# Kernel optimization log

Measured on AMD Instinct MI355X. Metric: run time of the kernel, lower is better.

## Reference

```python
import jax, jax.numpy as jnp
import numpy as np

ALPHA = 0.2  # LeakyReLU negative slope used by GAT attention


def _seg_softmax(scores, rows, n):
    # numerically stable softmax of per-edge scores grouped by destination row
    m = jax.ops.segment_max(scores, rows, num_segments=n)
    ex = jnp.exp(scores - m[rows])
    s = jax.ops.segment_sum(ex, rows, num_segments=n)
    return ex / s[rows]


def setup_inputs() -> dict:
    key = jax.random.key(0)
    ks = jax.random.split(key, 10)
    VOCAB, U, N, DEG = 200000, 50000, 20000, 16
    DIN, DOUT, H, ETYPES, EDIM = 64, 64, 4, 32, 64
    node_features = jax.random.normal(ks[0], (VOCAB, DIN), jnp.float32)
    W = jax.random.normal(ks[1], (H, DIN, DOUT), jnp.float32) * np.float32(np.sqrt(2.0 / (DIN + DOUT)))
    a_pos = jax.random.normal(ks[2], (H, 2 * DOUT), jnp.float32) * 0.1
    a_neg = jax.random.normal(ks[3], (H, 2 * DOUT), jnp.float32) * 0.1
    edge_embedding = jax.random.normal(ks[4], (ETYPES, EDIM), jnp.float32)
    edge_transform = jax.random.normal(ks[5], (EDIM, DOUT), jnp.float32) * np.float32(np.sqrt(2.0 / (EDIM + DOUT)))
    unique_nodes = jax.random.randint(ks[6], (U,), 0, VOCAB)
    row_unique = jax.random.randint(ks[7], (N,), 0, U)  # index of each output row's own node in the unique list
    # pos adjacency with self edges appended (adj_pos2 in the source)
    pos_row = jnp.concatenate([jnp.repeat(jnp.arange(N), DEG), jnp.arange(N)])
    pos_col = jnp.concatenate([jax.random.randint(ks[8], (N * DEG,), 0, U), row_unique])
    neg_row = jnp.repeat(jnp.arange(N), DEG)
    neg_col = jax.random.randint(ks[9], (N * DEG,), 0, U)
    return {
        "node_features": node_features, "W": W, "a_pos": a_pos, "a_neg": a_neg,
        "edge_embedding": edge_embedding, "edge_transform": edge_transform,
        "unique_nodes": unique_nodes, "row_unique": row_unique,
        "pos_row": pos_row, "pos_col": pos_col, "neg_row": neg_row, "neg_col": neg_col,
        "n_rows": N,
    }


def reference(node_features, W, a_pos, a_neg, edge_embedding, edge_transform,
              unique_nodes, row_unique, pos_row, pos_col, neg_row, neg_col, n_rows):
    embed = node_features[unique_nodes]                 # [U, Din] gather of unique node embeddings
    Wh = jnp.einsum('ud,hdo->huo', embed, W)            # [H, U, Dout]
    Dout = W.shape[-1]
    rows_all = jnp.concatenate([pos_row, neg_row])
    cols_all = jnp.concatenate([pos_col, neg_col])

    def head(Wh_h, ap, an):
        # per-node score halves (GAT trick: a^T[h_i || h_j] = a_dst.h_i + a_src.h_j)
        dst_p = (Wh_h @ ap[:Dout])[row_unique]          # [N]
        src_p = Wh_h @ ap[Dout:]                        # [U]
        dst_n = (Wh_h @ an[:Dout])[row_unique]
        src_n = Wh_h @ an[Dout:]
        e_pos = jax.nn.leaky_relu(dst_p[pos_row] + src_p[pos_col], ALPHA)
        e_neg = jax.nn.leaky_relu(dst_n[neg_row] + src_n[neg_col], ALPHA)
        att = _seg_softmax(jnp.concatenate([e_pos, e_neg]), rows_all, n_rows)  # joint softmax over pos+neg edges
        return jax.ops.segment_sum(att[:, None] * Wh_h[cols_all], rows_all, num_segments=n_rows)

    outs = jax.vmap(head)(Wh, a_pos, a_neg)             # [H, N, Dout]
    h_hidden = jax.nn.relu(jnp.transpose(outs, (1, 0, 2)).reshape(outs.shape[1], -1))  # concat heads -> ReLU
    edge_out = edge_embedding @ edge_transform          # edge-type projection
    return (h_hidden, edge_out)
```

## Files before the change

### kernel.cpp

```cpp
#include <hip/hip_runtime.h>
#include <hip/hip_bf16.h>
#include <hip/hip_fp16.h>
#include <math.h>

#define LRELU_ALPHA 0.2f

typedef __attribute__((ext_vector_type(8))) short bf16x8;
typedef __attribute__((ext_vector_type(4))) float f32x4;
typedef _Float16 f16x8 __attribute__((ext_vector_type(8)));

__device__ __forceinline__ unsigned short f2bf(float f) {
    union { float f; unsigned u; } v; v.f = f;
    unsigned r = v.u + 0x7fffu + ((v.u >> 16) & 1u);
    return (unsigned short)(r >> 16);
}
__device__ __forceinline__ unsigned short f2h(float f) {
    union { __half h; unsigned short s; } c; c.h = __float2half_rn(f); return c.s;
}
__device__ __forceinline__ unsigned cvtpk(float lo, float hi) {
    unsigned r;
    asm("v_cvt_pk_bf16_f32 %0, %1, %2" : "=v"(r) : "v"(lo), "v"(hi));
    return r;
}
__device__ __forceinline__ __half2 u2h2(unsigned u) {
    union { unsigned u; __half2 h; } x; x.u = u; return x.h;
}
__device__ __forceinline__ unsigned h22u(__half2 h) {
    union { __half2 h; unsigned u; } x; x.h = h; return x.u;
}

__global__ void prep_kernel(const float* __restrict__ W,
                            const float* __restrict__ a_pos, const float* __restrict__ a_neg,
                            const float* __restrict__ ee, const float* __restrict__ et,
                            unsigned short* __restrict__ Wt, unsigned short* __restrict__ avB,
                            float* __restrict__ edge_out, int H, int ET) {
    const int HE = H * 4096, AV = H * 256;
    int t = blockIdx.x * blockDim.x + threadIdx.x;
    if (t < HE) {
        int k = t & 63, n = (t >> 6) & 63, h = t >> 12;
        Wt[((size_t)h * 64 + n) * 64 + k] = f2h(W[(size_t)h * 4096 + k * 64 + n]);
    } else if (t < HE + AV) {
        int s = t - HE;
        int k = s & 63, q = (s >> 6) & 3, h = s >> 8;
        const float* a  = (q < 2 ? a_pos : a_neg) + (size_t)h * 128 + (q & 1) * 64;
        const float* wr = W + (size_t)h * 4096 + k * 64;
        float v = 0.f;
#pragma unroll
        for (int o = 0; o < 64; o += 4) {
            const float4 wv = *(const float4*)(wr + o);
            const float4 av = *(const float4*)(a + o);
            v = fmaf(wv.x, av.x, fmaf(wv.y, av.y, fmaf(wv.z, av.z, fmaf(wv.w, av.w, v))));
        }
        avB[((size_t)h * 4 + q) * 64 + k] = f2bf(v);
    } else {
        int s = t - HE - AV;
        if (s < ET * 64) {
            int e = s >> 6, o = s & 63;
            float acc = 0.f;
#pragma unroll
            for (int k = 0; k < 64; ++k)
                acc = fmaf(ee[e * 64 + k], et[k * 64 + o], acc);
            edge_out[s] = acc;
        }
    }
}

__global__ __launch_bounds__(256) void score_cvt_kernel(
    const float* __restrict__ nf, const unsigned short* __restrict__ avB,
    const int* __restrict__ un, unsigned short* __restrict__ embed16,
    float2* __restrict__ sc_dst, float2* __restrict__ sc_src, int U)
{
    const int wave = threadIdx.x >> 6;
    const int lane = threadIdx.x & 63;
    const int grp  = lane >> 4;
    const int r    = lane & 15;
    const long u0  = (long)blockIdx.x * 64 + wave * 16;
    if (u0 >= U) return;
    const long u  = u0 + r;
    const long ur = (u < U) ? u : (long)(U - 1);

    const float* erow = nf + (size_t)un[ur] * 64 + grp * 8;
    const float4 e0 = *(const float4*)(erow);
    const float4 e1 = *(const float4*)(erow + 4);
    const float4 e2 = *(const float4*)(erow + 32);
    const float4 e3 = *(const float4*)(erow + 36);

    union { unsigned d[4]; bf16x8 v; } A0, A1;
    A0.d[0] = cvtpk(e0.x, e0.y); A0.d[1] = cvtpk(e0.z, e0.w);
    A0.d[2] = cvtpk(e1.x, e1.y); A0.d[3] = cvtpk(e1.z, e1.w);
    A1.d[0] = cvtpk(e2.x, e2.y); A1.d[1] = cvtpk(e2.z, e2.w);
    A1.d[2] = cvtpk(e3.x, e3.y); A1.d[3] = cvtpk(e3.z, e3.w);

    if (u < U) {
        union { __half2 h2[4]; uint4 v; } F0, F1;
        F0.h2[0] = __floats2half2_rn(e0.x, e0.y); F0.h2[1] = __floats2half2_rn(e0.z, e0.w);
        F0.h2[2] = __floats2half2_rn(e1.x, e1.y); F0.h2[3] = __floats2half2_rn(e1.z, e1.w);
        F1.h2[0] = __floats2half2_rn(e2.x, e2.y); F1.h2[1] = __floats2half2_rn(e2.z, e2.w);
        F1.h2[2] = __floats2half2_rn(e3.x, e3.y); F1.h2[3] = __floats2half2_rn(e3.z, e3.w);
        *(uint4*)(embed16 + (size_t)u * 64 + grp * 8)      = F0.v;
        *(uint4*)(embed16 + (size_t)u * 64 + 32 + grp * 8) = F1.v;
    }

    f32x4 acc = (f32x4)(0.f);
    const unsigned short* wp = avB + (size_t)r * 64 + grp * 8;
    bf16x8 b0 = *(const bf16x8*)wp;
    bf16x8 b1 = *(const bf16x8*)(wp + 32);
    acc = __builtin_amdgcn_mfma_f32_16x16x32_bf16(b0, A0.v, acc, 0, 0, 0);
    acc = __builtin_amdgcn_mfma_f32_16x16x32_bf16(b1, A1.v, acc, 0, 0, 0);

    if (u < U) {
        sc_dst[(size_t)u * 4 + grp] = make_float2(acc[0], acc[2]);
        sc_src[(size_t)u * 4 + grp] = make_float2(acc[1], acc[3]);
    }
}

__global__ __launch_bounds__(512) void aggemm_kernel(
    const int* __restrict__ pos_col, const int* __restrict__ neg_col,
    const unsigned short* __restrict__ embed16,
    const float2* __restrict__ sc_dst, const float2* __restrict__ sc_src,
    const unsigned short* __restrict__ Wt,
    float* __restrict__ out, int N, int U)
{
    constexpr int DP = 16, NE = 33, NEP = 36;
    __shared__ int   s_col[8][2][NEP];
    __shared__ uint4 s_att[8][2][NEP];
    __shared__ __align__(16) unsigned short s_agg[16][256];

    const int wave = threadIdx.x >> 6;
    const int lane = threadIdx.x & 63;
    const int iA = blockIdx.x * 16 + wave * 2;
    const int iB = iA + 1;

    int colA = 0, colB = 0;
    if (lane < DP)       { colA = pos_col[(size_t)iA * DP + lane];
                           colB = pos_col[(size_t)iB * DP + lane]; }
    else if (lane == DP) { colA = pos_col[(size_t)N * DP + iA];
                           colB = pos_col[(size_t)N * DP + iB]; }
    else if (lane < NE)  { colA = neg_col[(size_t)iA * 16 + (lane - DP - 1)];
                           colB = neg_col[(size_t)iB * 16 + (lane - DP - 1)]; }

    const float4* ssv = (const float4*)sc_src;
    const float4 sA0 = ssv[2 * (size_t)(unsigned)colA];
    const float4 sA1 = ssv[2 * (size_t)(unsigned)colA + 1];
    const float4 sB0 = ssv[2 * (size_t)(unsigned)colB];
    const float4 sB1 = ssv[2 * (size_t)(unsigned)colB + 1];
    const int uA = __shfl(colA, DP, 64), uB = __shfl(colB, DP, 64);
    const float4* sdv = (const float4*)sc_dst;
    const float4 dA0 = sdv[2 * (size_t)(unsigned)uA];
    const float4 dA1 = sdv[2 * (size_t)(unsigned)uA + 1];
    const float4 dB0 = sdv[2 * (size_t)(unsigned)uB];
    const float4 dB1 = sdv[2 * (size_t)(unsigned)uB + 1];

    const bool isp = (lane <= DP);
    float a_s0 = isp ? dA0.x + sA0.x : dA0.y + sA0.y;
    float a_s1 = isp ? dA0.z + sA0.z : dA0.w + sA0.w;
    float a_s2 = isp ? dA1.x + sA1.x : dA1.y + sA1.y;
    float a_s3 = isp ? dA1.z + sA1.z : dA1.w + sA1.w;
    float b_s0 = isp ? dB0.x + sB0.x : dB0.y + sB0.y;
    float b_s1 = isp ? dB0.z + sB0.z : dB0.w + sB0.w;
    float b_s2 = isp ? dB1.x + sB1.x : dB1.y + sB1.y;
    float b_s3 = isp ? dB1.z + sB1.z : dB1.w + sB1.w;
    a_s0 = (a_s0 > 0.f) ? a_s0 : LRELU_ALPHA * a_s0;
    a_s1 = (a_s1 > 0.f) ? a_s1 : LRELU_ALPHA * a_s1;
    a_s2 = (a_s2 > 0.f) ? a_s2 : LRELU_ALPHA * a_s2;
    a_s3 = (a_s3 > 0.f) ? a_s3 : LRELU_ALPHA * a_s3;
    b_s0 = (b_s0 > 0.f) ? b_s0 : LRELU_ALPHA * b_s0;
    b_s1 = (b_s1 > 0.f) ? b_s1 : LRELU_ALPHA * b_s1;
    b_s2 = (b_s2 > 0.f) ? b_s2 : LRELU_ALPHA * b_s2;
    b_s3 = (b_s3 > 0.f) ? b_s3 : LRELU_ALPHA * b_s3;

    const bool act = (lane < NE);
    float ax0 = act ? __expf(a_s0) : 0.f, ax1 = act ? __expf(a_s1) : 0.f;
    float ax2 = act ? __expf(a_s2) : 0.f, ax3 = act ? __expf(a_s3) : 0.f;
    float bx0 = act ? __expf(b_s0) : 0.f, bx1 = act ? __expf(b_s1) : 0.f;
    float bx2 = act ? __expf(b_s2) : 0.f, bx3 = act ? __expf(b_s3) : 0.f;
    float aS0 = ax0, aS1 = ax1, aS2 = ax2, aS3 = ax3;
    float bS0 = bx0, bS1 = bx1, bS2 = bx2, bS3 = bx3;
#pragma unroll
    for (int off = 32; off; off >>= 1) {
        aS0 += __shfl_xor(aS0, off, 64); aS1 += __shfl_xor(aS1, off, 64);
        aS2 += __shfl_xor(aS2, off, 64); aS3 += __shfl_xor(aS3, off, 64);
        bS0 += __shfl_xor(bS0, off, 64); bS1 += __shfl_xor(bS1, off, 64);
        bS2 += __shfl_xor(bS2, off, 64); bS3 += __shfl_xor(bS3, off, 64);
    }
    if (lane < NEP) {
        uint4 tA, tB;
        tA.x = h22u(__float2half2_rn(__fdividef(ax0, aS0)));
        tA.y = h22u(__float2half2_rn(__fdividef(ax1, aS1)));
        tA.z = h22u(__float2half2_rn(__fdividef(ax2, aS2)));
        tA.w = h22u(__float2half2_rn(__fdividef(ax3, aS3)));
        tB.x = h22u(__float2half2_rn(__fdividef(bx0, bS0)));
        tB.y = h22u(__float2half2_rn(__fdividef(bx1, bS1)));
        tB.z = h22u(__float2half2_rn(__fdividef(bx2, bS2)));
        tB.w = h22u(__float2half2_rn(__fdividef(bx3, bS3)));
        s_col[wave][0][lane] = colA;  s_att[wave][0][lane] = tA;
        s_col[wave][1][lane] = colB;  s_att[wave][1][lane] = tB;
    }

    const int sub = lane >> 4;
    const int c   = lane & 15;
    const char* eb = (const char*)embed16 + (c << 3);
    __half2 accA[4][2], accB[4][2];
#pragma unroll
    for (int h = 0; h < 4; ++h)
        for (int d = 0; d < 2; ++d) {
            accA[h][d] = __float2half2_rn(0.f);
            accB[h][d] = __float2half2_rn(0.f);
        }
#pragma unroll
    for (int t = 0; t < 9; ++t) {
        const int   e  = 4 * t + sub;
        const int   cA = s_col[wave][0][e];
        const int   cB = s_col[wave][1][e];
        const uint2 vA = *(const uint2*)(eb + ((size_t)(unsigned)cA << 7));
        const uint2 vB = *(const uint2*)(eb + ((size_t)(unsigned)cB << 7));
        const uint4 tA = s_att[wave][0][e];
        const uint4 tB = s_att[wave][1][e];
        const __half2 vA0 = u2h2(vA.x), vA1 = u2h2(vA.y);
        const __half2 vB0 = u2h2(vB.x), vB1 = u2h2(vB.y);
        accA[0][0] = __hfma2(u2h2(tA.x), vA0, accA[0][0]);
        accA[0][1] = __hfma2(u2h2(tA.x), vA1, accA[0][1]);
        accA[1][0] = __hfma2(u2h2(tA.y), vA0, accA[1][0]);
        accA[1][1] = __hfma2(u2h2(tA.y), vA1, accA[1][1]);
        accA[2][0] = __hfma2(u2h2(tA.z), vA0, accA[2][0]);
        accA[2][1] = __hfma2(u2h2(tA.z), vA1, accA[2][1]);
        accA[3][0] = __hfma2(u2h2(tA.w), vA0, accA[3][0]);
        accA[3][1] = __hfma2(u2h2(tA.w), vA1, accA[3][1]);
        accB[0][0] = __hfma2(u2h2(tB.x), vB0, accB[0][0]);
        accB[0][1] = __hfma2(u2h2(tB.x), vB1, accB[0][1]);
        accB[1][0] = __hfma2(u2h2(tB.y), vB0, accB[1][0]);
        accB[1][1] = __hfma2(u2h2(tB.y), vB1, accB[1][1]);
        accB[2][0] = __hfma2(u2h2(tB.z), vB0, accB[2][0]);
        accB[2][1] = __hfma2(u2h2(tB.z), vB1, accB[2][1]);
        accB[3][0] = __hfma2(u2h2(tB.w), vB0, accB[3][0]);
        accB[3][1] = __hfma2(u2h2(tB.w), vB1, accB[3][1]);
    }
#pragma unroll
    for (int h = 0; h < 4; ++h)
#pragma unroll
        for (int d = 0; d < 2; ++d) {
            unsigned ua = h22u(accA[h][d]);
            ua = h22u(__hadd2(u2h2(ua), u2h2(__shfl_xor((int)ua, 16, 64))));
            ua = h22u(__hadd2(u2h2(ua), u2h2(__shfl_xor((int)ua, 32, 64))));
            accA[h][d] = u2h2(ua);
            unsigned ub = h22u(accB[h][d]);
            ub = h22u(__hadd2(u2h2(ub), u2h2(__shfl_xor((int)ub, 16, 64))));
            ub = h22u(__hadd2(u2h2(ub), u2h2(__shfl_xor((int)ub, 32, 64))));
            accB[h][d] = u2h2(ub);
        }
    if (sub == 0) {
#pragma unroll
        for (int h = 0; h < 4; ++h) {
            uint2 wA, wB;
            wA.x = h22u(accA[h][0]); wA.y = h22u(accA[h][1]);
            wB.x = h22u(accB[h][0]); wB.y = h22u(accB[h][1]);
            *(uint2*)((char*)&s_agg[wave * 2][h * 64] + c * 8)     = wA;
            *(uint2*)((char*)&s_agg[wave * 2 + 1][h * 64] + c * 8) = wB;
        }
    }
    __syncthreads();

    if (wave < 4) {
        const int h   = wave;
        const int grp = lane >> 4;
        const int r   = lane & 15;
        const f16x8 a0 = *(const f16x8*)((const char*)&s_agg[r][h * 64] + grp * 16);
        const f16x8 a1 = *(const f16x8*)((const char*)&s_agg[r][h * 64 + 32] + grp * 16);
        f32x4 acc[4];
#pragma unroll
        for (int nt = 0; nt < 4; ++nt) {
            acc[nt] = (f32x4)(0.f);
            const unsigned short* wp = Wt + (((size_t)h * 64 + nt * 16 + r) * 64 + grp * 8);
            const f16x8 b0 = *(const f16x8*)wp;
            const f16x8 b1 = *(const f16x8*)(wp + 32);
            acc[nt] = __builtin_amdgcn_mfma_f32_16x16x32_f16(b0, a0, acc[nt], 0, 0, 0);
            acc[nt] = __builtin_amdgcn_mfma_f32_16x16x32_f16(b1, a1, acc[nt], 0, 0, 0);
        }
        float* orow = out + ((size_t)(blockIdx.x * 16 + r) * 4 + h) * 64;
#pragma unroll
        for (int nt = 0; nt < 4; ++nt) {
            float4 o;
            o.x = fmaxf(acc[nt][0], 0.f); o.y = fmaxf(acc[nt][1], 0.f);
            o.z = fmaxf(acc[nt][2], 0.f); o.w = fmaxf(acc[nt][3], 0.f);
            *(float4*)(orow + nt * 16 + grp * 4) = o;
        }
    }
}

__global__ void embed_cvt_generic(const float* __restrict__ nf, const int* __restrict__ un,
                                  unsigned short* __restrict__ embed16, int U) {
    long t = (long)blockIdx.x * blockDim.x + threadIdx.x;
    if (t >= (long)U * 64) return;
    embed16[t] = f2h(nf[(size_t)un[t >> 6] * 64 + (t & 63)]);
}
__global__ void score_generic(const unsigned short* __restrict__ embed16,
                              const unsigned short* __restrict__ avB,
                              float2* __restrict__ sc_dst, float2* __restrict__ sc_src,
                              int U, int H) {
    long t = (long)blockIdx.x * blockDim.x + threadIdx.x;
    if (t >= (long)U * H) return;
    const long u = t / H; const int h = (int)(t % H);
    float s[4];
    for (int q = 0; q < 4; ++q) {
        float acc = 0.f;
        for (int k = 0; k < 64; ++k) {
            union { unsigned short s; __half h; } w; w.s = embed16[u * 64 + k];
            union { unsigned u; float f; } b; b.u = ((unsigned)avB[((size_t)h * 4 + q) * 64 + k]) << 16;
            acc = fmaf(__half2float(w.h), b.f, acc);
        }
        s[q] = acc;
    }
    sc_dst[u * H + h] = make_float2(s[0], s[2]);
    sc_src[u * H + h] = make_float2(s[1], s[3]);
}
__global__ __launch_bounds__(256) void agg_generic(
    const int* __restrict__ pos_col, const int* __restrict__ neg_col,
    const unsigned short* __restrict__ embed16,
    const float2* __restrict__ sc_dst, const float2* __restrict__ sc_src,
    unsigned short* __restrict__ aggb, int N, int U, int DEGP, int DEGN, int H)
{
    const int wave = threadIdx.x >> 6;
    const int lane = threadIdx.x & 63;
    const long j = (long)blockIdx.x * 4 + wave;
    const int i = (int)(j % N);
    const int h = (int)(j / N);
    if (h >= H) return;
    const int NE = DEGP + 1 + DEGN;

    int col = 0;
    if (lane < DEGP)       col = pos_col[(size_t)i * DEGP + lane];
    else if (lane == DEGP) col = pos_col[(size_t)N * DEGP + i];
    else if (lane < NE)    col = neg_col[(size_t)i * DEGN + (lane - DEGP - 1)];
    const float2 ss = sc_src[(size_t)col * H + h];
    const int u0s = __shfl(col, DEGP, 64);
    const float2 sd = sc_dst[(size_t)u0s * H + h];
    float score = -INFINITY;
    if (lane < NE) {
        const float raw = (lane <= DEGP) ? sd.x + ss.x : sd.y + ss.y;
        score = (raw > 0.f) ? raw : LRELU_ALPHA * raw;
    }
    float m = score;
#pragma unroll
    for (int off = 32; off; off >>= 1) m = fmaxf(m, __shfl_xor(m, off, 64));
    const float ex = (lane < NE) ? __expf(score - m) : 0.f;
    float S = ex;
#pragma unroll
    for (int off = 32; off; off >>= 1) S += __shfl_xor(S, off, 64);
    const float att = __fdividef(ex, S);

    float acc = 0.f;
    for (int e = 0; e < NE; ++e) {
        const int   ce = __shfl(col, e, 64);
        const float ae = __shfl(att, e, 64);
        union { unsigned short s; __half h; } w; w.s = embed16[(size_t)(unsigned)ce * 64 + lane];
        acc = fmaf(ae, __half2float(w.h), acc);
    }
    aggb[((size_t)i * H + h) * 64 + lane] = f2h(acc);
}
__global__ __launch_bounds__(256) void out_gemm_generic(
    const unsigned short* __restrict__ aggb, const unsigned short* __restrict__ Wt,
    float* __restrict__ out, int N, int H)
{
    const int wave = threadIdx.x >> 6;
    const int lane = threadIdx.x & 63;
    const int grp  = lane >> 4;
    const int r    = lane & 15;
    const long j = (long)blockIdx.x * 4 + wave;
    const int  h = (int)(j % H);
    const long i0 = (j / H) * 16;
    if (i0 >= N) return;
    const long i  = i0 + r;
    const long ir = (i < N) ? i : (long)(N - 1);

    const unsigned short* arow = aggb + ((size_t)ir * H + h) * 64 + grp * 8;
    const f16x8 a0 = *(const f16x8*)arow;
    const f16x8 a1 = *(const f16x8*)(arow + 32);
    f32x4 acc[4];
#pragma unroll
    for (int nt = 0; nt < 4; ++nt) {
        acc[nt] = (f32x4)(0.f);
        const unsigned short* wp = Wt + (((size_t)h * 64 + nt * 16 + r) * 64 + grp * 8);
        const f16x8 b0 = *(const f16x8*)wp;
        const f16x8 b1 = *(const f16x8*)(wp + 32);
        acc[nt] = __builtin_amdgcn_mfma_f32_16x16x32_f16(b0, a0, acc[nt], 0, 0, 0);
        acc[nt] = __builtin_amdgcn_mfma_f32_16x16x32_f16(b1, a1, acc[nt], 0, 0, 0);
    }
    if (i < N) {
        float* orow = out + ((size_t)i * H + h) * 64;
#pragma unroll
        for (int nt = 0; nt < 4; ++nt) {
            float4 o;
            o.x = fmaxf(acc[nt][0], 0.f); o.y = fmaxf(acc[nt][1], 0.f);
            o.z = fmaxf(acc[nt][2], 0.f); o.w = fmaxf(acc[nt][3], 0.f);
            *(float4*)(orow + nt * 16 + grp * 4) = o;
        }
    }
}

extern "C" void kernel_launch(void* const* d_in, const int* in_sizes, int n_in,
                              void* d_out, int out_size, void* d_ws, size_t ws_size,
                              hipStream_t stream) {
    const float* nf     = (const float*)d_in[0];
    const float* W      = (const float*)d_in[1];
    const float* a_pos  = (const float*)d_in[2];
    const float* a_neg  = (const float*)d_in[3];
    const float* ee     = (const float*)d_in[4];
    const float* et     = (const float*)d_in[5];
    const int* unique_nodes = (const int*)d_in[6];
    const int* pos_col  = (const int*)d_in[9];
    const int* neg_col  = (const int*)d_in[11];

    const int U    = in_sizes[6];
    const int N    = in_sizes[7];
    const int Epos = in_sizes[8];
    const int Eneg = in_sizes[10];
    const int H    = in_sizes[1] / (64 * 64);
    const int DEGN = Eneg / N;
    const int DEGP = Epos / N - 1;
    const int ET   = in_sizes[4] / 64;

    char* ws = (char*)d_ws;
    auto alloc = [&](size_t bytes) { char* p = ws; ws += (bytes + 255) & ~(size_t)255; return p; };
    unsigned short* embed16 = (unsigned short*)alloc((size_t)U * 64 * 2);
    float2*         sc_dst  = (float2*)alloc((size_t)U * H * 8);
    float2*         sc_src  = (float2*)alloc((size_t)U * H * 8);
    unsigned short* aggb    = (unsigned short*)alloc((size_t)N * H * 64 * 2);
    unsigned short* Wt      = (unsigned short*)alloc((size_t)H * 4096 * 2);
    unsigned short* avB     = (unsigned short*)alloc((size_t)H * 256 * 2);
    float* out = (float*)d_out;

    const int PT = H * 4096 + H * 256 + ET * 64;
    prep_kernel<<<(PT + 255) / 256, 256, 0, stream>>>(W, a_pos, a_neg, ee, et, Wt, avB,
                                                      out + (size_t)N * H * 64, H, ET);

    if (H == 4 && DEGP == 16 && DEGN == 16 && (N % 16) == 0) {
        score_cvt_kernel<<<(U + 63) / 64, 256, 0, stream>>>(nf, avB, unique_nodes,
                                                            embed16, sc_dst, sc_src, U);
        aggemm_kernel<<<N / 16, 512, 0, stream>>>(pos_col, neg_col, embed16,
                                                  sc_dst, sc_src, Wt, out, N, U);
    } else {
        embed_cvt_generic<<<(int)(((long)U * 64 + 255) / 256), 256, 0, stream>>>(
            nf, unique_nodes, embed16, U);
        score_generic<<<(int)(((long)U * H + 255) / 256), 256, 0, stream>>>(
            embed16, avB, sc_dst, sc_src, U, H);
        agg_generic<<<(int)(((long)N * H + 3) / 4), 256, 0, stream>>>(
            pos_col, neg_col, embed16, sc_dst, sc_src, aggb, N, U, DEGP, DEGN, H);
        const long tiles = ((long)N + 15) / 16;
        out_gemm_generic<<<(int)((tiles * H + 3) / 4), 256, 0, stream>>>(aggb, Wt, out, N, H);
    }
}
```

Before: 47.57 us.

## Broadcast edge columns and attention via shuffles, widen gathers to 16 bytes, swizzle LDS

Drops the per-wave shared-memory staging of edge column indices and attention weights; each lane now fetches them straight from the producing lanes with __shfl. The gather loop splits the 64-wide row into 8 chunks of 16 bytes instead of 16 chunks of 8 bytes, so there are 5 iterations of wider loads rather than 9, at the cost of one extra shuffle-reduction step. The aggregate tile in LDS gets an XOR swizzle to reduce bank conflicts when the MFMA stage reads it. In exchange the loop issues more cross-lane shuffles, the accumulator arrays double in size, and the iteration count is padded to 40 edge slots.

```diff
diff --git a/kernel.cpp b/kernel.cpp
--- a/kernel.cpp
+++ b/kernel.cpp
@@ -121,9 +121,7 @@
     const unsigned short* __restrict__ Wt,
     float* __restrict__ out, int N, int U)
 {
-    constexpr int DP = 16, NE = 33, NEP = 36;
-    __shared__ int   s_col[8][2][NEP];
-    __shared__ uint4 s_att[8][2][NEP];
+    constexpr int DP = 16, NE = 33;
     __shared__ __align__(16) unsigned short s_agg[16][256];
 
     const int wave = threadIdx.x >> 6;
@@ -183,79 +181,74 @@
         bS0 += __shfl_xor(bS0, off, 64); bS1 += __shfl_xor(bS1, off, 64);
         bS2 += __shfl_xor(bS2, off, 64); bS3 += __shfl_xor(bS3, off, 64);
     }
-    if (lane < NEP) {
-        uint4 tA, tB;
-        tA.x = h22u(__float2half2_rn(__fdividef(ax0, aS0)));
-        tA.y = h22u(__float2half2_rn(__fdividef(ax1, aS1)));
-        tA.z = h22u(__float2half2_rn(__fdividef(ax2, aS2)));
-        tA.w = h22u(__float2half2_rn(__fdividef(ax3, aS3)));
-        tB.x = h22u(__float2half2_rn(__fdividef(bx0, bS0)));
-        tB.y = h22u(__float2half2_rn(__fdividef(bx1, bS1)));
-        tB.z = h22u(__float2half2_rn(__fdividef(bx2, bS2)));
-        tB.w = h22u(__float2half2_rn(__fdividef(bx3, bS3)));
-        s_col[wave][0][lane] = colA;  s_att[wave][0][lane] = tA;
-        s_col[wave][1][lane] = colB;  s_att[wave][1][lane] = tB;
-    }
-
-    const int sub = lane >> 4;
-    const int c   = lane & 15;
-    const char* eb = (const char*)embed16 + (c << 3);
-    __half2 accA[4][2], accB[4][2];
+    unsigned aA[4], aB[4];
+    aA[0] = h22u(__float2half2_rn(__fdividef(ax0, aS0)));
+    aA[1] = h22u(__float2half2_rn(__fdividef(ax1, aS1)));
+    aA[2] = h22u(__float2half2_rn(__fdividef(ax2, aS2)));
+    aA[3] = h22u(__float2half2_rn(__fdividef(ax3, aS3)));
+    aB[0] = h22u(__float2half2_rn(__fdividef(bx0, bS0)));
+    aB[1] = h22u(__float2half2_rn(__fdividef(bx1, bS1)));
+    aB[2] = h22u(__float2half2_rn(__fdividef(bx2, bS2)));
+    aB[3] = h22u(__float2half2_rn(__fdividef(bx3, bS3)));
+
+    const int sub = lane >> 3;
+    const int c   = lane & 7;
+    const char* eb = (const char*)embed16 + (c << 4);
+    __half2 accA[4][4], accB[4][4];
 #pragma unroll
     for (int h = 0; h < 4; ++h)
-        for (int d = 0; d < 2; ++d) {
+#pragma unroll
+        for (int d = 0; d < 4; ++d) {
             accA[h][d] = __float2half2_rn(0.f);
             accB[h][d] = __float2half2_rn(0.f);
         }
 #pragma unroll
-    for (int t = 0; t < 9; ++t) {
-        const int   e  = 4 * t + sub;
-        const int   cA = s_col[wave][0][e];
-        const int   cB = s_col[wave][1][e];
-        const uint2 vA = *(const uint2*)(eb + ((size_t)(unsigned)cA << 7));
-        const uint2 vB = *(const uint2*)(eb + ((size_t)(unsigned)cB << 7));
-        const uint4 tA = s_att[wave][0][e];
-        const uint4 tB = s_att[wave][1][e];
-        const __half2 vA0 = u2h2(vA.x), vA1 = u2h2(vA.y);
-        const __half2 vB0 = u2h2(vB.x), vB1 = u2h2(vB.y);
-        accA[0][0] = __hfma2(u2h2(tA.x), vA0, accA[0][0]);
-        accA[0][1] = __hfma2(u2h2(tA.x), vA1, accA[0][1]);
-        accA[1][0] = __hfma2(u2h2(tA.y), vA0, accA[1][0]);
-        accA[1][1] = __hfma2(u2h2(tA.y), vA1, accA[1][1]);
-        accA[2][0] = __hfma2(u2h2(tA.z), vA0, accA[2][0]);
-        accA[2][1] = __hfma2(u2h2(tA.z), vA1, accA[2][1]);
-        accA[3][0] = __hfma2(u2h2(tA.w), vA0, accA[3][0]);
-        accA[3][1] = __hfma2(u2h2(tA.w), vA1, accA[3][1]);
-        accB[0][0] = __hfma2(u2h2(tB.x), vB0, accB[0][0]);
-        accB[0][1] = __hfma2(u2h2(tB.x), vB1, accB[0][1]);
-        accB[1][0] = __hfma2(u2h2(tB.y), vB0, accB[1][0]);
-        accB[1][1] = __hfma2(u2h2(tB.y), vB1, accB[1][1]);
-        accB[2][0] = __hfma2(u2h2(tB.z), vB0, accB[2][0]);
-        accB[2][1] = __hfma2(u2h2(tB.z), vB1, accB[2][1]);
-        accB[3][0] = __hfma2(u2h2(tB.w), vB0, accB[3][0]);
-        accB[3][1] = __hfma2(u2h2(tB.w), vB1, accB[3][1]);
+    for (int t = 0; t < 5; ++t) {
+        const int e  = 8 * t + sub;
+        const int cA = __shfl(colA, e, 64);
+        const int cB = __shfl(colB, e, 64);
+        const uint4 vA = *(const uint4*)(eb + ((size_t)(unsigned)cA << 7));
+        const uint4 vB = *(const uint4*)(eb + ((size_t)(unsigned)cB << 7));
+#pragma unroll
+        for (int h = 0; h < 4; ++h) {
+            const __half2 tA = u2h2((unsigned)__shfl((int)aA[h], e, 64));
+            const __half2 tB = u2h2((unsigned)__shfl((int)aB[h], e, 64));
+            accA[h][0] = __hfma2(tA, u2h2(vA.x), accA[h][0]);
+            accA[h][1] = __hfma2(tA, u2h2(vA.y), accA[h][1]);
+            accA[h][2] = __hfma2(tA, u2h2(vA.z), accA[h][2]);
+            accA[h][3] = __hfma2(tA, u2h2(vA.w), accA[h][3]);
+            accB[h][0] = __hfma2(tB, u2h2(vB.x), accB[h][0]);
+            accB[h][1] = __hfma2(tB, u2h2(vB.y), accB[h][1]);
+            accB[h][2] = __hfma2(tB, u2h2(vB.z), accB[h][2]);
+            accB[h][3] = __hfma2(tB, u2h2(vB.w), accB[h][3]);
+        }
     }
 #pragma unroll
     for (int h = 0; h < 4; ++h)
 #pragma unroll
-        for (int d = 0; d < 2; ++d) {
+        for (int d = 0; d < 4; ++d) {
             unsigned ua = h22u(accA[h][d]);
-            ua = h22u(__hadd2(u2h2(ua), u2h2(__shfl_xor((int)ua, 16, 64))));
-            ua = h22u(__hadd2(u2h2(ua), u2h2(__shfl_xor((int)ua, 32, 64))));
+            ua = h22u(__hadd2(u2h2(ua), u2h2((unsigned)__shfl_xor((int)ua, 8, 64))));
+            ua = h22u(__hadd2(u2h2(ua), u2h2((unsigned)__shfl_xor((int)ua, 16, 64))));
+            ua = h22u(__hadd2(u2h2(ua), u2h2((unsigned)__shfl_xor((int)ua, 32, 64))));
             accA[h][d] = u2h2(ua);
             unsigned ub = h22u(accB[h][d]);
-            ub = h22u(__hadd2(u2h2(ub), u2h2(__shfl_xor((int)ub, 16, 64))));
-            ub = h22u(__hadd2(u2h2(ub), u2h2(__shfl_xor((int)ub, 32, 64))));
+            ub = h22u(__hadd2(u2h2(ub), u2h2((unsigned)__shfl_xor((int)ub, 8, 64))));
+            ub = h22u(__hadd2(u2h2(ub), u2h2((unsigned)__shfl_xor((int)ub, 16, 64))));
+            ub = h22u(__hadd2(u2h2(ub), u2h2((unsigned)__shfl_xor((int)ub, 32, 64))));
             accB[h][d] = u2h2(ub);
         }
     if (sub == 0) {
+        const int rA = wave * 2, rB = rA + 1;
 #pragma unroll
         for (int h = 0; h < 4; ++h) {
-            uint2 wA, wB;
+            uint4 wA, wB;
             wA.x = h22u(accA[h][0]); wA.y = h22u(accA[h][1]);
+            wA.z = h22u(accA[h][2]); wA.w = h22u(accA[h][3]);
             wB.x = h22u(accB[h][0]); wB.y = h22u(accB[h][1]);
-            *(uint2*)((char*)&s_agg[wave * 2][h * 64] + c * 8)     = wA;
-            *(uint2*)((char*)&s_agg[wave * 2 + 1][h * 64] + c * 8) = wB;
+            wB.z = h22u(accB[h][2]); wB.w = h22u(accB[h][3]);
+            *(uint4*)((char*)&s_agg[rA][0] + h * 128 + ((c ^ (rA & 7)) << 4)) = wA;
+            *(uint4*)((char*)&s_agg[rB][0] + h * 128 + ((c ^ (rB & 7)) << 4)) = wB;
         }
     }
     __syncthreads();
@@ -264,8 +257,9 @@
         const int h   = wave;
         const int grp = lane >> 4;
         const int r   = lane & 15;
-        const f16x8 a0 = *(const f16x8*)((const char*)&s_agg[r][h * 64] + grp * 16);
-        const f16x8 a1 = *(const f16x8*)((const char*)&s_agg[r][h * 64 + 32] + grp * 16);
+        const char* arow = (const char*)&s_agg[r][0] + h * 128;
+        const f16x8 a0 = *(const f16x8*)(arow + ((grp       ^ (r & 7)) << 4));
+        const f16x8 a1 = *(const f16x8*)(arow + (((4 + grp) ^ (r & 7)) << 4));
         f32x4 acc[4];
 #pragma unroll
         for (int nt = 0; nt < 4; ++nt) {
```

After: 51.66 us. 1.09x slower.

## Split fp16 embedding table into low/high halves and aggregate in two passes

Applied to the files above, without the earlier changes.

The fp16 embedding table is stored as two separate 64-byte-per-row arrays (dims 0-31 and 32-63). The aggregation gathers each half in its own pass, with 8 lanes per edge instead of 16, so each pass's working set is half the size and is more likely to stay in cache. In exchange it adds a second pass with an extra shuffle-reduction stage and an extra block barrier. Padding the edge lists to 40 entries means 7 wasted edge slots are processed per pass instead of 3.

```diff
diff --git a/kernel.cpp b/kernel.cpp
--- a/kernel.cpp
+++ b/kernel.cpp
@@ -67,7 +67,8 @@
 
 __global__ __launch_bounds__(256) void score_cvt_kernel(
     const float* __restrict__ nf, const unsigned short* __restrict__ avB,
-    const int* __restrict__ un, unsigned short* __restrict__ embed16,
+    const int* __restrict__ un, unsigned short* __restrict__ elo,
+    unsigned short* __restrict__ ehi,
     float2* __restrict__ sc_dst, float2* __restrict__ sc_src, int U)
 {
     const int wave = threadIdx.x >> 6;
@@ -97,8 +98,8 @@
         F0.h2[2] = __floats2half2_rn(e1.x, e1.y); F0.h2[3] = __floats2half2_rn(e1.z, e1.w);
         F1.h2[0] = __floats2half2_rn(e2.x, e2.y); F1.h2[1] = __floats2half2_rn(e2.z, e2.w);
         F1.h2[2] = __floats2half2_rn(e3.x, e3.y); F1.h2[3] = __floats2half2_rn(e3.z, e3.w);
-        *(uint4*)(embed16 + (size_t)u * 64 + grp * 8)      = F0.v;
-        *(uint4*)(embed16 + (size_t)u * 64 + 32 + grp * 8) = F1.v;
+        *(uint4*)(elo + (size_t)u * 32 + grp * 8) = F0.v;
+        *(uint4*)(ehi + (size_t)u * 32 + grp * 8) = F1.v;
     }
 
     f32x4 acc = (f32x4)(0.f);
@@ -116,12 +117,12 @@
 
 __global__ __launch_bounds__(512) void aggemm_kernel(
     const int* __restrict__ pos_col, const int* __restrict__ neg_col,
-    const unsigned short* __restrict__ embed16,
+    const unsigned short* __restrict__ elo, const unsigned short* __restrict__ ehi,
     const float2* __restrict__ sc_dst, const float2* __restrict__ sc_src,
     const unsigned short* __restrict__ Wt,
     float* __restrict__ out, int N, int U)
 {
-    constexpr int DP = 16, NE = 33, NEP = 36;
+    constexpr int DP = 16, NE = 33, NEP = 40;
     __shared__ int   s_col[8][2][NEP];
     __shared__ uint4 s_att[8][2][NEP];
     __shared__ __align__(16) unsigned short s_agg[16][256];
@@ -197,75 +198,82 @@
         s_col[wave][1][lane] = colB;  s_att[wave][1][lane] = tB;
     }
 
-    const int sub = lane >> 4;
-    const int c   = lane & 15;
-    const char* eb = (const char*)embed16 + (c << 3);
-    __half2 accA[4][2], accB[4][2];
-#pragma unroll
-    for (int h = 0; h < 4; ++h)
-        for (int d = 0; d < 2; ++d) {
-            accA[h][d] = __float2half2_rn(0.f);
-            accB[h][d] = __float2half2_rn(0.f);
-        }
-#pragma unroll
-    for (int t = 0; t < 9; ++t) {
-        const int   e  = 4 * t + sub;
-        const int   cA = s_col[wave][0][e];
-        const int   cB = s_col[wave][1][e];
-        const uint2 vA = *(const uint2*)(eb + ((size_t)(unsigned)cA << 7));
-        const uint2 vB = *(const uint2*)(eb + ((size_t)(unsigned)cB << 7));
-        const uint4 tA = s_att[wave][0][e];
-        const uint4 tB = s_att[wave][1][e];
-        const __half2 vA0 = u2h2(vA.x), vA1 = u2h2(vA.y);
-        const __half2 vB0 = u2h2(vB.x), vB1 = u2h2(vB.y);
-        accA[0][0] = __hfma2(u2h2(tA.x), vA0, accA[0][0]);
-        accA[0][1] = __hfma2(u2h2(tA.x), vA1, accA[0][1]);
-        accA[1][0] = __hfma2(u2h2(tA.y), vA0, accA[1][0]);
-        accA[1][1] = __hfma2(u2h2(tA.y), vA1, accA[1][1]);
-        accA[2][0] = __hfma2(u2h2(tA.z), vA0, accA[2][0]);
-        accA[2][1] = __hfma2(u2h2(tA.z), vA1, accA[2][1]);
-        accA[3][0] = __hfma2(u2h2(tA.w), vA0, accA[3][0]);
-        accA[3][1] = __hfma2(u2h2(tA.w), vA1, accA[3][1]);
-        accB[0][0] = __hfma2(u2h2(tB.x), vB0, accB[0][0]);
-        accB[0][1] = __hfma2(u2h2(tB.x), vB1, accB[0][1]);
-        accB[1][0] = __hfma2(u2h2(tB.y), vB0, accB[1][0]);
-        accB[1][1] = __hfma2(u2h2(tB.y), vB1, accB[1][1]);
-        accB[2][0] = __hfma2(u2h2(tB.z), vB0, accB[2][0]);
-        accB[2][1] = __hfma2(u2h2(tB.z), vB1, accB[2][1]);
-        accB[3][0] = __hfma2(u2h2(tB.w), vB0, accB[3][0]);
-        accB[3][1] = __hfma2(u2h2(tB.w), vB1, accB[3][1]);
-    }
-#pragma unroll
-    for (int h = 0; h < 4; ++h)
-#pragma unroll
-        for (int d = 0; d < 2; ++d) {
-            unsigned ua = h22u(accA[h][d]);
-            ua = h22u(__hadd2(u2h2(ua), u2h2(__shfl_xor((int)ua, 16, 64))));
-            ua = h22u(__hadd2(u2h2(ua), u2h2(__shfl_xor((int)ua, 32, 64))));
-            accA[h][d] = u2h2(ua);
-            unsigned ub = h22u(accB[h][d]);
-            ub = h22u(__hadd2(u2h2(ub), u2h2(__shfl_xor((int)ub, 16, 64))));
-            ub = h22u(__hadd2(u2h2(ub), u2h2(__shfl_xor((int)ub, 32, 64))));
-            accB[h][d] = u2h2(ub);
-        }
-    if (sub == 0) {
-#pragma unroll
-        for (int h = 0; h < 4; ++h) {
-            uint2 wA, wB;
-            wA.x = h22u(accA[h][0]); wA.y = h22u(accA[h][1]);
-            wB.x = h22u(accB[h][0]); wB.y = h22u(accB[h][1]);
-            *(uint2*)((char*)&s_agg[wave * 2][h * 64] + c * 8)     = wA;
-            *(uint2*)((char*)&s_agg[wave * 2 + 1][h * 64] + c * 8) = wB;
-        }
-    }
-    __syncthreads();
+    const int sub = lane >> 3;
+    const int c   = lane & 7;
+    const int rA  = wave * 2, rB = rA + 1;
+#pragma unroll
+    for (int half = 0; half < 2; ++half) {
+        const char* eb = (const char*)(half ? ehi : elo) + (c << 3);
+        __half2 accA[4][2], accB[4][2];
+#pragma unroll
+        for (int h = 0; h < 4; ++h)
+#pragma unroll
+            for (int d = 0; d < 2; ++d) {
+                accA[h][d] = __float2half2_rn(0.f);
+                accB[h][d] = __float2half2_rn(0.f);
+            }
+#pragma unroll
+        for (int t = 0; t < 5; ++t) {
+            const int e  = 8 * t + sub;
+            const int cA = s_col[wave][0][e];
+            const int cB = s_col[wave][1][e];
+            const uint2 vA = *(const uint2*)(eb + ((size_t)(unsigned)cA << 6));
+            const uint2 vB = *(const uint2*)(eb + ((size_t)(unsigned)cB << 6));
+            const uint4 aA = s_att[wave][0][e];
+            const uint4 aB = s_att[wave][1][e];
+            const __half2 vA0 = u2h2(vA.x), vA1 = u2h2(vA.y);
+            const __half2 vB0 = u2h2(vB.x), vB1 = u2h2(vB.y);
+            accA[0][0] = __hfma2(u2h2(aA.x), vA0, accA[0][0]);
+            accA[0][1] = __hfma2(u2h2(aA.x), vA1, accA[0][1]);
+            accA[1][0] = __hfma2(u2h2(aA.y), vA0, accA[1][0]);
+            accA[1][1] = __hfma2(u2h2(aA.y), vA1, accA[1][1]);
+            accA[2][0] = __hfma2(u2h2(aA.z), vA0, accA[2][0]);
+            accA[2][1] = __hfma2(u2h2(aA.z), vA1, accA[2][1]);
+            accA[3][0] = __hfma2(u2h2(aA.w), vA0, accA[3][0]);
+            accA[3][1] = __hfma2(u2h2(aA.w), vA1, accA[3][1]);
+            accB[0][0] = __hfma2(u2h2(aB.x), vB0, accB[0][0]);
+            accB[0][1] = __hfma2(u2h2(aB.x), vB1, accB[0][1]);
+            accB[1][0] = __hfma2(u2h2(aB.y), vB0, accB[1][0]);
+            accB[1][1] = __hfma2(u2h2(aB.y), vB1, accB[1][1]);
+            accB[2][0] = __hfma2(u2h2(aB.z), vB0, accB[2][0]);
+            accB[2][1] = __hfma2(u2h2(aB.z), vB1, accB[2][1]);
+            accB[3][0] = __hfma2(u2h2(aB.w), vB0, accB[3][0]);
+            accB[3][1] = __hfma2(u2h2(aB.w), vB1, accB[3][1]);
+        }
+#pragma unroll
+        for (int h = 0; h < 4; ++h)
+#pragma unroll
+            for (int d = 0; d < 2; ++d) {
+                unsigned ua = h22u(accA[h][d]);
+                ua = h22u(__hadd2(u2h2(ua), u2h2((unsigned)__shfl_xor((int)ua, 8, 64))));
+                ua = h22u(__hadd2(u2h2(ua), u2h2((unsigned)__shfl_xor((int)ua, 16, 64))));
+                ua = h22u(__hadd2(u2h2(ua), u2h2((unsigned)__shfl_xor((int)ua, 32, 64))));
+                accA[h][d] = u2h2(ua);
+                unsigned ub = h22u(accB[h][d]);
+                ub = h22u(__hadd2(u2h2(ub), u2h2((unsigned)__shfl_xor((int)ub, 8, 64))));
+                ub = h22u(__hadd2(u2h2(ub), u2h2((unsigned)__shfl_xor((int)ub, 16, 64))));
+                ub = h22u(__hadd2(u2h2(ub), u2h2((unsigned)__shfl_xor((int)ub, 32, 64))));
+                accB[h][d] = u2h2(ub);
+            }
+        if (sub == 0) {
+#pragma unroll
+            for (int h = 0; h < 4; ++h) {
+                uint2 wA, wB;
+                wA.x = h22u(accA[h][0]); wA.y = h22u(accA[h][1]);
+                wB.x = h22u(accB[h][0]); wB.y = h22u(accB[h][1]);
+                *(uint2*)((char*)&s_agg[rA][0] + h * 128 + half * 64 + (c << 3)) = wA;
+                *(uint2*)((char*)&s_agg[rB][0] + h * 128 + half * 64 + (c << 3)) = wB;
+            }
+        }
+        __syncthreads();
+    }
 
     if (wave < 4) {
         const int h   = wave;
         const int grp = lane >> 4;
         const int r   = lane & 15;
-        const f16x8 a0 = *(const f16x8*)((const char*)&s_agg[r][h * 64] + grp * 16);
-        const f16x8 a1 = *(const f16x8*)((const char*)&s_agg[r][h * 64 + 32] + grp * 16);
+        const f16x8 a0 = *(const f16x8*)((const char*)&s_agg[r][0] + h * 128 + grp * 16);
+        const f16x8 a1 = *(const f16x8*)((const char*)&s_agg[r][0] + h * 128 + 64 + grp * 16);
         f32x4 acc[4];
 #pragma unroll
         for (int nt = 0; nt < 4; ++nt) {
@@ -288,12 +296,23 @@
 }
 
 __global__ void embed_cvt_generic(const float* __restrict__ nf, const int* __restrict__ un,
-                                  unsigned short* __restrict__ embed16, int U) {
+                                  unsigned short* __restrict__ elo,
+                                  unsigned short* __restrict__ ehi, int U) {
     long t = (long)blockIdx.x * blockDim.x + threadIdx.x;
     if (t >= (long)U * 64) return;
-    embed16[t] = f2h(nf[(size_t)un[t >> 6] * 64 + (t & 63)]);
-}
-__global__ void score_generic(const unsigned short* __restrict__ embed16,
+    const long u = t >> 6; const int dim = (int)(t & 63);
+    const unsigned short v = f2h(nf[(size_t)un[u] * 64 + dim]);
+    if (dim < 32) elo[u * 32 + dim] = v;
+    else          ehi[u * 32 + dim - 32] = v;
+}
+__device__ __forceinline__ float emb_at(const unsigned short* elo, const unsigned short* ehi,
+                                        long u, int k) {
+    union { unsigned short s; __half h; } w;
+    w.s = (k < 32) ? elo[u * 32 + k] : ehi[u * 32 + k - 32];
+    return __half2float(w.h);
+}
+__global__ void score_generic(const unsigned short* __restrict__ elo,
+                              const unsigned short* __restrict__ ehi,
                               const unsigned short* __restrict__ avB,
                               float2* __restrict__ sc_dst, float2* __restrict__ sc_src,
                               int U, int H) {
@@ -304,9 +323,9 @@
     for (int q = 0; q < 4; ++q) {
         float acc = 0.f;
         for (int k = 0; k < 64; ++k) {
-            union { unsigned short s; __half h; } w; w.s = embed16[u * 64 + k];
-            union { unsigned u; float f; } b; b.u = ((unsigned)avB[((size_t)h * 4 + q) * 64 + k]) << 16;
-            acc = fmaf(__half2float(w.h), b.f, acc);
+            union { unsigned uu; float f; } b;
+            b.uu = ((unsigned)avB[((size_t)h * 4 + q) * 64 + k]) << 16;
+            acc = fmaf(emb_at(elo, ehi, u, k), b.f, acc);
         }
         s[q] = acc;
     }
@@ -315,7 +334,7 @@
 }
 __global__ __launch_bounds__(256) void agg_generic(
     const int* __restrict__ pos_col, const int* __restrict__ neg_col,
-    const unsigned short* __restrict__ embed16,
+    const unsigned short* __restrict__ elo, const unsigned short* __restrict__ ehi,
     const float2* __restrict__ sc_dst, const float2* __restrict__ sc_src,
     unsigned short* __restrict__ aggb, int N, int U, int DEGP, int DEGN, int H)
 {
@@ -352,8 +371,7 @@
     for (int e = 0; e < NE; ++e) {
         const int   ce = __shfl(col, e, 64);
         const float ae = __shfl(att, e, 64);
-        union { unsigned short s; __half h; } w; w.s = embed16[(size_t)(unsigned)ce * 64 + lane];
-        acc = fmaf(ae, __half2float(w.h), acc);
+        acc = fmaf(ae, emb_at(elo, ehi, (long)(unsigned)ce, lane), acc);
     }
     aggb[((size_t)i * H + h) * 64 + lane] = f2h(acc);
 }
@@ -421,12 +439,13 @@
 
     char* ws = (char*)d_ws;
     auto alloc = [&](size_t bytes) { char* p = ws; ws += (bytes + 255) & ~(size_t)255; return p; };
-    unsigned short* embed16 = (unsigned short*)alloc((size_t)U * 64 * 2);
-    float2*         sc_dst  = (float2*)alloc((size_t)U * H * 8);
-    float2*         sc_src  = (float2*)alloc((size_t)U * H * 8);
-    unsigned short* aggb    = (unsigned short*)alloc((size_t)N * H * 64 * 2);
-    unsigned short* Wt      = (unsigned short*)alloc((size_t)H * 4096 * 2);
-    unsigned short* avB     = (unsigned short*)alloc((size_t)H * 256 * 2);
+    unsigned short* elo    = (unsigned short*)alloc((size_t)U * 32 * 2);
+    unsigned short* ehi    = (unsigned short*)alloc((size_t)U * 32 * 2);
+    float2*         sc_dst = (float2*)alloc((size_t)U * H * 8);
+    float2*         sc_src = (float2*)alloc((size_t)U * H * 8);
+    unsigned short* aggb   = (unsigned short*)alloc((size_t)N * H * 64 * 2);
+    unsigned short* Wt     = (unsigned short*)alloc((size_t)H * 4096 * 2);
+    unsigned short* avB    = (unsigned short*)alloc((size_t)H * 256 * 2);
     float* out = (float*)d_out;
 
     const int PT = H * 4096 + H * 256 + ET * 64;
@@ -435,16 +454,16 @@
 
     if (H == 4 && DEGP == 16 && DEGN == 16 && (N % 16) == 0) {
         score_cvt_kernel<<<(U + 63) / 64, 256, 0, stream>>>(nf, avB, unique_nodes,
-                                                            embed16, sc_dst, sc_src, U);
-        aggemm_kernel<<<N / 16, 512, 0, stream>>>(pos_col, neg_col, embed16,
+                                                            elo, ehi, sc_dst, sc_src, U);
+        aggemm_kernel<<<N / 16, 512, 0, stream>>>(pos_col, neg_col, elo, ehi,
                                                   sc_dst, sc_src, Wt, out, N, U);
     } else {
         embed_cvt_generic<<<(int)(((long)U * 64 + 255) / 256), 256, 0, stream>>>(
-            nf, unique_nodes, embed16, U);
+            nf, unique_nodes, elo, ehi, U);
         score_generic<<<(int)(((long)U * H + 255) / 256), 256, 0, stream>>>(
-            embed16, avB, sc_dst, sc_src, U, H);
+            elo, ehi, avB, sc_dst, sc_src, U, H);
         agg_generic<<<(int)(((long)N * H + 3) / 4), 256, 0, stream>>>(
-            pos_col, neg_col, embed16, sc_dst, sc_src, aggb, N, U, DEGP, DEGN, H);
+            pos_col, neg_col, elo, ehi, sc_dst, sc_src, aggb, N, U, DEGP, DEGN, H);
         const long tiles = ((long)N + 15) / 16;
         out_gemm_generic<<<(int)((tiles * H + 3) / 4), 256, 0, stream>>>(aggb, Wt, out, N, H);
     }
```

New measurement: 50.27 us. 5.7% more time.
